# Performance work log

Hardware: AMD Instinct MI355X
Metric: run time of the kernel (lower is better)

Reference implementation:

```python
import jax, jax.numpy as jnp
import numpy as np

LATENT = 1024
HID = 512
J = 24
# SMPL kinematic tree (parent[0] = -1 is the root, unused in the loop)
PARENT = [-1, 0, 0, 0, 1, 2, 3, 4, 5, 6, 7, 8, 9, 9, 9, 12, 13, 14, 16, 17, 18, 19, 20, 21]
EPS = 1e-12  # F.normalize default eps


def setup_inputs() -> dict:
    key = jax.random.key(0)
    k1, k2, k3, k4, k5 = jax.random.split(key, 5)
    B = 32768
    # Kaiming-uniform-ish init scales for the Linear layers
    s1 = 1.0 / np.sqrt(LATENT)
    s2 = 1.0 / np.sqrt(HID)
    return {
        "z": jax.random.normal(k1, (B, LATENT), dtype=jnp.float32),
        "W1": jax.random.uniform(k2, (LATENT, HID), minval=-s1, maxval=s1, dtype=jnp.float32),
        "b1": jax.random.uniform(k3, (HID,), minval=-s1, maxval=s1, dtype=jnp.float32),
        "W2": jax.random.uniform(k4, (HID, (J - 1) * 4), minval=-s2, maxval=s2, dtype=jnp.float32),
        "b2": jax.random.uniform(k5, ((J - 1) * 4,), minval=-s2, maxval=s2, dtype=jnp.float32),
    }


def reference(z, W1, b1, W2, b2):
    B = z.shape[0]
    h = jax.nn.silu(z @ W1 + b1)                    # [B, 512]
    raw = (h @ W2 + b2).reshape(B, J - 1, 4)        # [B, J-1, 4]
    vec = raw[..., :3]                              # [B, J-1, 3]
    norm = jnp.linalg.norm(vec, axis=-1, keepdims=True)
    direction = vec / jnp.maximum(norm, EPS)        # F.normalize(dim=-1)
    length = jax.nn.softplus(raw[..., 3])           # [B, J-1]
    child_off = direction * length[..., None]       # [B, J-1, 3]
    offsets = jnp.concatenate(
        [jnp.zeros((B, 1, 3), dtype=z.dtype), child_off], axis=1
    )                                                # [B, J, 3]
    # Static-tree forward kinematics: unroll the (small, fixed) joint loop.
    joints_list = [jnp.zeros((B, 3), dtype=z.dtype)]
    for j in range(1, J):
        joints_list.append(joints_list[PARENT[j]] + offsets[:, j])
    joints = jnp.stack(joints_list, axis=1)          # [B, J, 3]
    return (joints, offsets, length)
```

## Files before the change

### kernel.cpp

```cpp
#include <hip/hip_runtime.h>
#include <hip/hip_bf16.h>
#include <stdint.h>

#define BROWS 32768
#define LATENT 1024
#define HID 512

typedef float f32x4 __attribute__((ext_vector_type(4)));
typedef __bf16 bf16x8 __attribute__((ext_vector_type(8)));
typedef unsigned short us8 __attribute__((ext_vector_type(8)));

__device__ __forceinline__ void gload16(const void* g, void* l) {
  __builtin_amdgcn_global_load_lds(
      (__attribute__((address_space(1))) void*)g,
      (__attribute__((address_space(3))) void*)l, 16, 0, 0);
}

__device__ __forceinline__ void split_bf16(float x, unsigned short& hi, unsigned short& lo) {
  __bf16 h = (__bf16)x;
  float r = x - (float)h;
  __bf16 l = (__bf16)r;
  hi = __builtin_bit_cast(unsigned short, h);
  lo = __builtin_bit_cast(unsigned short, l);
}

__device__ __forceinline__ f32x4 mfma16(bf16x8 a, bf16x8 b, f32x4 c) {
  return __builtin_amdgcn_mfma_f32_16x16x32_bf16(a, b, c, 0, 0, 0);
}

__device__ __forceinline__ bf16x8 ldfrag(const void* p) {
  return __builtin_bit_cast(bf16x8, *(const us8*)p);
}

__global__ __launch_bounds__(256) void k_prep_w1f(const float* __restrict__ W1,
                                                  unsigned short* __restrict__ w1f) {
  const int n = blockIdx.x;
  const int t = threadIdx.x;
  const int kt = t >> 3, ls = t & 7;
  const int p = ls ^ (n & 7);
  const int k0 = kt * 32 + (ls & 3) * 8;
  unsigned short v[8];
#pragma unroll
  for (int e = 0; e < 8; e++) {
    const float x = W1[(size_t)(k0 + e) * HID + n];
    unsigned short h, q;
    split_bf16(x, h, q);
    v[e] = (ls < 4) ? h : q;
  }
  unsigned short* dst = w1f + ((size_t)n * 32 + kt) * 64 + p * 8;
  *(ushort4*)(dst) = make_ushort4(v[0], v[1], v[2], v[3]);
  *(ushort4*)(dst + 4) = make_ushort4(v[4], v[5], v[6], v[7]);
}

__global__ __launch_bounds__(256) void k_prep_w2t(const float* __restrict__ W2,
                                                  unsigned short* __restrict__ hi,
                                                  unsigned short* __restrict__ lo) {
  const int idx = blockIdx.x * 256 + threadIdx.x;
  const int n = idx >> 9, k = idx & 511;
  const float v = (n < 92) ? W2[(size_t)k * 92 + n] : 0.0f;
  unsigned short h, l;
  split_bf16(v, h, l);
  hi[idx] = h;
  lo[idx] = l;
}

__global__ __launch_bounds__(512, 2) void k_gemm1(
    const float* __restrict__ z, const unsigned short* __restrict__ w1f,
    const float* __restrict__ b1,
    unsigned short* __restrict__ hh, unsigned short* __restrict__ hl) {
  extern __shared__ __align__(16) char lb[];

  const int tid = threadIdx.x;
  const int bid = blockIdx.x;
  const int swz = (bid & 7) * 64 + (bid >> 3);
  const int mb = swz >> 1, nbk = swz & 1;
  const int m0 = mb * 128, n0g = nbk * 256;

  const int wv = tid >> 6, l = tid & 63;
  const int wr = wv >> 2, wc = wv & 3;
  const int l15 = l & 15, lg = l >> 4;
  const int x7 = l15 & 7;

  const int rowAB = (wr * 64 + l15) * 128;
  const int sA0 = (((2 * lg) ^ x7)) << 4;
  const int sA1 = (((2 * lg + 1) ^ x7)) << 4;
  const int rowBB = 16384 + (wc * 64 + l15) * 128;
  const int sBH = ((lg ^ x7)) << 4;
  const int sBL = ((((4 | lg)) ^ x7)) << 4;

  const int lr = l >> 3, lc = l & 7;
  const char* zA0 = (const char*)z +
      ((size_t)(m0 + wv * 16 + lr)) * 4096 + ((lc ^ (lr & 7)) << 4);
  const char* zB0 = (const char*)w1f +
      ((size_t)(n0g + wv * 32 + lr)) * 4096 + (lc << 4);

  f32x4 acc[4][4] = {};
  f32x4 af[4][2];
  bf16x8 ah[4], al[4], bhf[4], blf[4];

#define STAGE(nbase, kt1)                                                     \
  {                                                                           \
    _Pragma("unroll") for (int j_ = 0; j_ < 2; j_++)                          \
        gload16(zA0 + (size_t)j_ * 32768 + (kt1) * 128,                       \
                lb + (nbase) + (wv * 2 + j_) * 1024);                         \
    _Pragma("unroll") for (int j_ = 0; j_ < 4; j_++)                          \
        gload16(zB0 + (size_t)j_ * 32768 + (kt1) * 128,                       \
                lb + (nbase) + 16384 + (wv * 4 + j_) * 1024);                 \
  }

#define LD_A(cb)                                                              \
  {                                                                           \
    _Pragma("unroll") for (int mf = 0; mf < 4; mf++) {                        \
      af[mf][0] = *(const f32x4*)(lb + (cb) + rowAB + mf * 2048 + sA0);       \
      af[mf][1] = *(const f32x4*)(lb + (cb) + rowAB + mf * 2048 + sA1);       \
    }                                                                         \
  }

#define LD_BH(cb)                                                             \
  {                                                                           \
    _Pragma("unroll") for (int nf = 0; nf < 4; nf++)                          \
        bhf[nf] = ldfrag(lb + (cb) + rowBB + nf * 2048 + sBH);                \
  }

#define LD_BL(cb)                                                             \
  {                                                                           \
    _Pragma("unroll") for (int nf = 0; nf < 4; nf++)                          \
        blf[nf] = ldfrag(lb + (cb) + rowBB + nf * 2048 + sBL);                \
  }

#define SPLIT_HI                                                              \
  {                                                                           \
    _Pragma("unroll") for (int mf = 0; mf < 4; mf++)                          \
        _Pragma("unroll") for (int e = 0; e < 4; e++) {                       \
      ah[mf][e] = (__bf16)af[mf][0][e];                                       \
      ah[mf][4 + e] = (__bf16)af[mf][1][e];                                   \
    }                                                                         \
  }

#define SPLIT_LO                                                              \
  {                                                                           \
    _Pragma("unroll") for (int mf = 0; mf < 4; mf++)                          \
        _Pragma("unroll") for (int e = 0; e < 4; e++) {                       \
      al[mf][e] = (__bf16)(af[mf][0][e] - (float)ah[mf][e]);                  \
      al[mf][4 + e] = (__bf16)(af[mf][1][e] - (float)ah[mf][4 + e]);          \
    }                                                                         \
  }

#define MCL(AF, BF)                                                           \
  {                                                                           \
    __builtin_amdgcn_s_setprio(1);                                            \
    _Pragma("unroll") for (int mf = 0; mf < 4; mf++)                          \
        _Pragma("unroll") for (int nf = 0; nf < 4; nf++)                      \
            acc[mf][nf] = mfma16(AF[mf], BF[nf], acc[mf][nf]);                \
    __builtin_amdgcn_s_setprio(0);                                            \
  }

#define SBAR { asm volatile("" ::: "memory"); __builtin_amdgcn_s_barrier();   \
               asm volatile("" ::: "memory"); }
#define VM0  asm volatile("s_waitcnt vmcnt(0)" ::: "memory")

  STAGE(0, 0);
  VM0;
  SBAR;
  LD_A(0);
  LD_BH(0);

#pragma unroll 2
  for (int t = 0; t < 32; ++t) {
    const int cb = (t & 1) * 49152;
    const int nb = cb ^ 49152;
    const bool pre = (t < 31);

    LD_BL(cb);
    if (pre) STAGE(nb, t + 1);
    SBAR;
    SPLIT_HI;
    MCL(ah, bhf);
    SBAR;

    SPLIT_LO;
    MCL(al, bhf);

    VM0;
    SBAR;
    MCL(ah, blf);
    if (pre) {
      LD_A(nb);
      LD_BH(nb);
    }
    SBAR;
  }

  float b1v[4];
#pragma unroll
  for (int nf = 0; nf < 4; nf++) b1v[nf] = b1[n0g + wc * 64 + nf * 16 + l15];

#pragma unroll
  for (int mf = 0; mf < 4; mf++)
#pragma unroll
    for (int nf = 0; nf < 4; nf++)
#pragma unroll
      for (int r = 0; r < 4; r++) {
        const int gm = m0 + wr * 64 + mf * 16 + (lg << 2) + r;
        const int gn = n0g + wc * 64 + nf * 16 + l15;
        const float x = acc[mf][nf][r] + b1v[nf];
        const float hval = x / (1.0f + expf(-x));
        unsigned short hi_, lo_;
        split_bf16(hval, hi_, lo_);
        const size_t o = (size_t)gm * HID + gn;
        hh[o] = hi_;
        hl[o] = lo_;
      }
}

__global__ __launch_bounds__(256, 2) void k_gemm2(
    const unsigned short* __restrict__ hh, const unsigned short* __restrict__ hl,
    const unsigned short* __restrict__ w2h, const unsigned short* __restrict__ w2l,
    const float* __restrict__ b2, float* __restrict__ out) {
  __shared__ unsigned short Ah[2][2048], Al[2][2048];
  __shared__ unsigned short Bh[2][4096], Bl[2][4096];
  __shared__ float raw[64][97];

  const int tid = threadIdx.x;
  const int m0 = blockIdx.x * 64;
  const int w = tid >> 6, lane = tid & 63;
  const int wr = w >> 1, wc = w & 1;
  const int l15 = lane & 15, lg = lane >> 4;
  const int arow = tid >> 2, ac8 = (tid & 3) << 3;

  const unsigned short* hhb = hh + (size_t)(m0 + arow) * HID + ac8;
  const unsigned short* hlb = hl + (size_t)(m0 + arow) * HID + ac8;
  const unsigned short* w2hb = w2h + (size_t)arow * HID + ac8;
  const unsigned short* w2lb = w2l + (size_t)arow * HID + ac8;

  f32x4 acc[2][3] = {};

#define G2_STAGE(kt, bf) { \
    gload16(hhb + (kt) * 32, &Ah[bf][(w << 9)]); \
    gload16(hlb + (kt) * 32, &Al[bf][(w << 9)]); \
    gload16(w2hb + (kt) * 32,            &Bh[bf][(w << 9)]); \
    gload16(w2hb + (kt) * 32 + 64 * HID, &Bh[bf][2048 + (w << 9)]); \
    gload16(w2lb + (kt) * 32,            &Bl[bf][(w << 9)]); \
    gload16(w2lb + (kt) * 32 + 64 * HID, &Bl[bf][2048 + (w << 9)]); }

#define G2_COMPUTE(bf) { \
    bf16x8 ah2[2], al2[2], bh2[3], bl2[3]; \
    _Pragma("unroll") \
    for (int mf = 0; mf < 2; mf++) { \
      const int o_ = ((wr * 32 + mf * 16 + l15) << 5) + (lg << 3); \
      ah2[mf] = ldfrag(&Ah[bf][o_]); \
      al2[mf] = ldfrag(&Al[bf][o_]); \
    } \
    _Pragma("unroll") \
    for (int nf = 0; nf < 3; nf++) { \
      const int o_ = ((wc * 48 + nf * 16 + l15) << 5) + (lg << 3); \
      bh2[nf] = ldfrag(&Bh[bf][o_]); \
      bl2[nf] = ldfrag(&Bl[bf][o_]); \
    } \
    _Pragma("unroll") \
    for (int mf = 0; mf < 2; mf++) { \
      _Pragma("unroll") \
      for (int nf = 0; nf < 3; nf++) { \
        acc[mf][nf] = mfma16(ah2[mf], bh2[nf], acc[mf][nf]); \
        acc[mf][nf] = mfma16(al2[mf], bh2[nf], acc[mf][nf]); \
        acc[mf][nf] = mfma16(ah2[mf], bl2[nf], acc[mf][nf]); \
      } } }

  G2_STAGE(0, 0);
  __syncthreads();
#pragma unroll 2
  for (int kt = 0; kt < 16; kt++) {
    const int cur = kt & 1, nx = cur ^ 1;
    if (kt < 15) G2_STAGE(kt + 1, nx);
    G2_COMPUTE(cur);
    __syncthreads();
  }

#pragma unroll
  for (int mf = 0; mf < 2; mf++) {
#pragma unroll
    for (int nf = 0; nf < 3; nf++) {
#pragma unroll
      for (int r = 0; r < 4; r++) {
        const int ml = wr * 32 + mf * 16 + (lg << 2) + r;
        const int nl = wc * 48 + nf * 16 + l15;
        raw[ml][nl] = acc[mf][nf][r];
      }
    }
  }
  __syncthreads();

  const size_t OFFB = (size_t)BROWS * 72;
  const size_t LENB = (size_t)BROWS * 144;

  for (int task = tid; task < 64 * 24; task += 256) {
    const int row = task / 24;
    const int j = task - row * 24;
    const int gm = m0 + row;
    float* orow = out + OFFB + (size_t)gm * 72;
    if (j == 0) {
      orow[0] = 0.0f; orow[1] = 0.0f; orow[2] = 0.0f;
    } else {
      const int c0 = (j - 1) * 4;
      const float vx = raw[row][c0 + 0] + b2[c0 + 0];
      const float vy = raw[row][c0 + 1] + b2[c0 + 1];
      const float vz = raw[row][c0 + 2] + b2[c0 + 2];
      const float wvv = raw[row][c0 + 3] + b2[c0 + 3];
      const float nrm = sqrtf(vx * vx + vy * vy + vz * vz);
      const float inv = 1.0f / fmaxf(nrm, 1e-12f);
      const float len = fmaxf(wvv, 0.0f) + log1pf(expf(-fabsf(wvv)));
      const float sc = inv * len;
      const float ox = vx * sc, oy = vy * sc, oz = vz * sc;
      orow[j * 3 + 0] = ox; orow[j * 3 + 1] = oy; orow[j * 3 + 2] = oz;
      out[LENB + (size_t)gm * 23 + (j - 1)] = len;
      raw[row][c0 + 0] = ox; raw[row][c0 + 1] = oy; raw[row][c0 + 2] = oz;
    }
  }
  __syncthreads();

  if (tid < 64) {
    constexpr int PAR[24] = {-1, 0, 0, 0, 1, 2, 3, 4, 5, 6, 7, 8,
                             9, 9, 9, 12, 13, 14, 16, 17, 18, 19, 20, 21};
    const int gm = m0 + tid;
    float e[72];
    e[0] = 0.0f; e[1] = 0.0f; e[2] = 0.0f;
#pragma unroll
    for (int j = 1; j < 24; j++) {
      const int p = PAR[j];
      const int c0 = (j - 1) * 4;
      e[3 * j + 0] = e[3 * p + 0] + raw[tid][c0 + 0];
      e[3 * j + 1] = e[3 * p + 1] + raw[tid][c0 + 1];
      e[3 * j + 2] = e[3 * p + 2] + raw[tid][c0 + 2];
    }
    float4* jo = (float4*)(out + (size_t)gm * 72);
#pragma unroll
    for (int q = 0; q < 18; q++)
      jo[q] = make_float4(e[4 * q + 0], e[4 * q + 1], e[4 * q + 2], e[4 * q + 3]);
  }
}

extern "C" void kernel_launch(void* const* d_in, const int* in_sizes, int n_in,
                              void* d_out, int out_size, void* d_ws, size_t ws_size,
                              hipStream_t stream) {
  const float* z = (const float*)d_in[0];
  const float* W1 = (const float*)d_in[1];
  const float* b1 = (const float*)d_in[2];
  const float* W2 = (const float*)d_in[3];
  const float* b2 = (const float*)d_in[4];
  float* out = (float*)d_out;

  char* ws = (char*)d_ws;
  unsigned short* w1f = (unsigned short*)(ws);
  unsigned short* w2h = (unsigned short*)(ws + (2 << 20));
  unsigned short* w2l = (unsigned short*)(ws + (2 << 20) + 131072);
  unsigned short* hh = (unsigned short*)(ws + ((size_t)4 << 20));
  unsigned short* hl = (unsigned short*)(ws + ((size_t)4 << 20) + ((size_t)32 << 20));

  hipFuncSetAttribute((const void*)k_gemm1,
                      hipFuncAttributeMaxDynamicSharedMemorySize, 98304);

  hipLaunchKernelGGL(k_prep_w1f, dim3(512), dim3(256), 0, stream, W1, w1f);
  hipLaunchKernelGGL(k_prep_w2t, dim3(256), dim3(256), 0, stream, W2, w2h, w2l);
  hipLaunchKernelGGL(k_gemm1, dim3(512), dim3(512), 98304, stream, z, w1f, b1, hh, hl);
  hipLaunchKernelGGL(k_gemm2, dim3(512), dim3(256), 0, stream, hh, hl, w2h, w2l, b2, out);
}
```

Baseline: 157.1 us.

## Pre-split A tile into bf16 hi/lo in LDS with smaller 128x128 blocks

The GEMM1 kernel now loads z through registers, splits it once into bf16 hi/lo and writes both halves to LDS. Each wave then reads ready bf16 fragments instead of every wave converting fp32 fragments itself. Tiles shrink from 128x256 with 512 threads to 128x128 with 256 threads, giving twice as many blocks and 64KB of LDS per block. The cost is that each z tile is now re-read by 4 column blocks instead of 2, and there are more barriers per k-step.

```diff
diff --git a/kernel.cpp b/kernel.cpp
--- a/kernel.cpp
+++ b/kernel.cpp
@@ -64,7 +64,7 @@
   lo[idx] = l;
 }
 
-__global__ __launch_bounds__(512, 2) void k_gemm1(
+__global__ __launch_bounds__(256, 2) void k_gemm1(
     const float* __restrict__ z, const unsigned short* __restrict__ w1f,
     const float* __restrict__ b1,
     unsigned short* __restrict__ hh, unsigned short* __restrict__ hl) {
@@ -72,78 +72,68 @@
 
   const int tid = threadIdx.x;
   const int bid = blockIdx.x;
-  const int swz = (bid & 7) * 64 + (bid >> 3);
-  const int mb = swz >> 1, nbk = swz & 1;
-  const int m0 = mb * 128, n0g = nbk * 256;
+  const int swz = (bid & 7) * 128 + (bid >> 3);
+  const int mb = swz >> 2, nbk = swz & 3;
+  const int m0 = mb * 128, n0g = nbk * 128;
 
   const int wv = tid >> 6, l = tid & 63;
-  const int wr = wv >> 2, wc = wv & 3;
+  const int wr = wv >> 1, wc = wv & 1;
   const int l15 = l & 15, lg = l >> 4;
   const int x7 = l15 & 7;
 
-  const int rowAB = (wr * 64 + l15) * 128;
-  const int sA0 = (((2 * lg) ^ x7)) << 4;
-  const int sA1 = (((2 * lg + 1) ^ x7)) << 4;
-  const int rowBB = 16384 + (wc * 64 + l15) * 128;
-  const int sBH = ((lg ^ x7)) << 4;
-  const int sBL = ((((4 | lg)) ^ x7)) << 4;
-
-  const int lr = l >> 3, lc = l & 7;
-  const char* zA0 = (const char*)z +
-      ((size_t)(m0 + wv * 16 + lr)) * 4096 + ((lc ^ (lr & 7)) << 4);
-  const char* zB0 = (const char*)w1f +
-      ((size_t)(n0g + wv * 32 + lr)) * 4096 + (lc << 4);
+  const int ahB = (wr * 64 + l15) * 128 + ((lg ^ x7) << 4);
+  const int alB = (wr * 64 + l15) * 128 + ((((4 | lg) ^ x7)) << 4);
+  const int bhB = 16384 + (wc * 64 + l15) * 128 + ((lg ^ x7) << 4);
+  const int blB = 16384 + (wc * 64 + l15) * 128 + ((((4 | lg) ^ x7)) << 4);
+
+  const int arow = tid >> 1;
+  const int k0a = (tid & 1) * 16;
+  const float* zsrc = z + (size_t)(m0 + arow) * LATENT + k0a;
+  int adst_hi[4], adst_lo[4];
+#pragma unroll
+  for (int q = 0; q < 4; q++) {
+    const int k = k0a + 4 * q;
+    const int sl = k >> 3, hf = ((k >> 2) & 1) * 8;
+    adst_hi[q] = arow * 128 + ((sl ^ (arow & 7)) << 4) + hf;
+    adst_lo[q] = arow * 128 + ((((4 | sl)) ^ (arow & 7)) << 4) + hf;
+  }
+
+  const unsigned short* bsrc =
+      w1f + ((size_t)(n0g + (tid >> 3)) * 32) * 64 + (tid & 7) * 8;
+  const int bdst = 16384 + (tid >> 3) * 128 + (tid & 7) * 16;
 
   f32x4 acc[4][4] = {};
-  f32x4 af[4][2];
-  bf16x8 ah[4], al[4], bhf[4], blf[4];
-
-#define STAGE(nbase, kt1)                                                     \
-  {                                                                           \
-    _Pragma("unroll") for (int j_ = 0; j_ < 2; j_++)                          \
-        gload16(zA0 + (size_t)j_ * 32768 + (kt1) * 128,                       \
-                lb + (nbase) + (wv * 2 + j_) * 1024);                         \
+  f32x4 ar[4];
+  bf16x8 ah[4], al[4], bh[4], bl[4];
+
+#define LOAD_A(kt1)                                                           \
+  {                                                                           \
+    _Pragma("unroll") for (int q = 0; q < 4; q++)                             \
+        ar[q] = *(const f32x4*)(zsrc + (kt1) * 32 + 4 * q);                   \
+  }
+
+#define GLOAD_B(nbase, kt1)                                                   \
+  {                                                                           \
     _Pragma("unroll") for (int j_ = 0; j_ < 4; j_++)                          \
-        gload16(zB0 + (size_t)j_ * 32768 + (kt1) * 128,                       \
-                lb + (nbase) + 16384 + (wv * 4 + j_) * 1024);                 \
-  }
-
-#define LD_A(cb)                                                              \
-  {                                                                           \
-    _Pragma("unroll") for (int mf = 0; mf < 4; mf++) {                        \
-      af[mf][0] = *(const f32x4*)(lb + (cb) + rowAB + mf * 2048 + sA0);       \
-      af[mf][1] = *(const f32x4*)(lb + (cb) + rowAB + mf * 2048 + sA1);       \
+        gload16(bsrc + (size_t)j_ * 65536 + (kt1) * 64,                       \
+                lb + (nbase) + bdst + j_ * 4096);                             \
+  }
+
+#define SPLIT_WRITE(nbase)                                                    \
+  {                                                                           \
+    _Pragma("unroll") for (int q = 0; q < 4; q++) {                           \
+      unsigned short h0, h1, h2, h3, q0, q1, q2, q3;                          \
+      split_bf16(ar[q][0], h0, q0); split_bf16(ar[q][1], h1, q1);             \
+      split_bf16(ar[q][2], h2, q2); split_bf16(ar[q][3], h3, q3);             \
+      *(ushort4*)(lb + (nbase) + adst_hi[q]) = make_ushort4(h0, h1, h2, h3);  \
+      *(ushort4*)(lb + (nbase) + adst_lo[q]) = make_ushort4(q0, q1, q2, q3);  \
     }                                                                         \
   }
 
-#define LD_BH(cb)                                                             \
-  {                                                                           \
-    _Pragma("unroll") for (int nf = 0; nf < 4; nf++)                          \
-        bhf[nf] = ldfrag(lb + (cb) + rowBB + nf * 2048 + sBH);                \
-  }
-
-#define LD_BL(cb)                                                             \
-  {                                                                           \
-    _Pragma("unroll") for (int nf = 0; nf < 4; nf++)                          \
-        blf[nf] = ldfrag(lb + (cb) + rowBB + nf * 2048 + sBL);                \
-  }
-
-#define SPLIT_HI                                                              \
-  {                                                                           \
-    _Pragma("unroll") for (int mf = 0; mf < 4; mf++)                          \
-        _Pragma("unroll") for (int e = 0; e < 4; e++) {                       \
-      ah[mf][e] = (__bf16)af[mf][0][e];                                       \
-      ah[mf][4 + e] = (__bf16)af[mf][1][e];                                   \
-    }                                                                         \
-  }
-
-#define SPLIT_LO                                                              \
-  {                                                                           \
-    _Pragma("unroll") for (int mf = 0; mf < 4; mf++)                          \
-        _Pragma("unroll") for (int e = 0; e < 4; e++) {                       \
-      al[mf][e] = (__bf16)(af[mf][0][e] - (float)ah[mf][e]);                  \
-      al[mf][4 + e] = (__bf16)(af[mf][1][e] - (float)ah[mf][4 + e]);          \
-    }                                                                         \
+#define LD4(dst, cb, base)                                                    \
+  {                                                                           \
+    _Pragma("unroll") for (int f_ = 0; f_ < 4; f_++)                          \
+        dst[f_] = ldfrag(lb + (cb) + (base) + f_ * 2048);                     \
   }
 
 #define MCL(AF, BF)                                                           \
@@ -155,39 +145,51 @@
     __builtin_amdgcn_s_setprio(0);                                            \
   }
 
-#define SBAR { asm volatile("" ::: "memory"); __builtin_amdgcn_s_barrier();   \
-               asm volatile("" ::: "memory"); }
-#define VM0  asm volatile("s_waitcnt vmcnt(0)" ::: "memory")
-
-  STAGE(0, 0);
+#define FENCE asm volatile("" ::: "memory")
+#define SBAR { FENCE; __builtin_amdgcn_s_barrier(); FENCE; }
+#define LGKM0 asm volatile("s_waitcnt lgkmcnt(0)" ::: "memory")
+#define VM4 asm volatile("s_waitcnt vmcnt(4)" ::: "memory")
+#define VM0 asm volatile("s_waitcnt vmcnt(0)" ::: "memory")
+
+  LOAD_A(0);
+  FENCE;
+  GLOAD_B(0, 0);
+  VM4;
+  SPLIT_WRITE(0);
   VM0;
+  LGKM0;
   SBAR;
-  LD_A(0);
-  LD_BH(0);
-
-#pragma unroll 2
+
   for (int t = 0; t < 32; ++t) {
-    const int cb = (t & 1) * 49152;
-    const int nb = cb ^ 49152;
+    const int cb = (t & 1) * 32768;
+    const int nb = cb ^ 32768;
     const bool pre = (t < 31);
 
-    LD_BL(cb);
-    if (pre) STAGE(nb, t + 1);
+    LD4(ah, cb, ahB);
+    LD4(bh, cb, bhB);
+    if (pre) {
+      LOAD_A(t + 1);
+      FENCE;
+      GLOAD_B(nb, t + 1);
+    }
+    SBAR; LGKM0;
+    MCL(ah, bh);
     SBAR;
-    SPLIT_HI;
-    MCL(ah, bhf);
+
+    LD4(al, cb, alB);
+    SBAR; LGKM0;
+    MCL(al, bh);
     SBAR;
 
-    SPLIT_LO;
-    MCL(al, bhf);
-
-    VM0;
+    LD4(bl, cb, blB);
+    if (pre) {
+      VM4;
+      SPLIT_WRITE(nb);
+      VM0;
+    }
+    LGKM0;
     SBAR;
-    MCL(ah, blf);
-    if (pre) {
-      LD_A(nb);
-      LD_BH(nb);
-    }
+    MCL(ah, bl);
     SBAR;
   }
 
@@ -357,10 +359,10 @@
   unsigned short* hl = (unsigned short*)(ws + ((size_t)4 << 20) + ((size_t)32 << 20));
 
   hipFuncSetAttribute((const void*)k_gemm1,
-                      hipFuncAttributeMaxDynamicSharedMemorySize, 98304);
+                      hipFuncAttributeMaxDynamicSharedMemorySize, 65536);
 
   hipLaunchKernelGGL(k_prep_w1f, dim3(512), dim3(256), 0, stream, W1, w1f);
   hipLaunchKernelGGL(k_prep_w2t, dim3(256), dim3(256), 0, stream, W2, w2h, w2l);
-  hipLaunchKernelGGL(k_gemm1, dim3(512), dim3(512), 98304, stream, z, w1f, b1, hh, hl);
+  hipLaunchKernelGGL(k_gemm1, dim3(1024), dim3(256), 65536, stream, z, w1f, b1, hh, hl);
   hipLaunchKernelGGL(k_gemm2, dim3(512), dim3(256), 0, stream, hh, hl, w2h, w2l, b2, out);
 }
```

Result: faster. 153.7 us (-2.2%).
